# Optimization experiments

Measured on AMD Instinct MI355X. Metric: run time of the kernel, lower is better.

Reference implementation:

```python
import jax, jax.numpy as jnp
import numpy as np

B, C, H, S, E, NH, DD, DS = 16, 256, 1024, 1024, 512, 8, 512, 64
HD = E // NH               # head dim = 64
REL_MAX = 2048             # seq_len + prediction_length
S1 = S + 1                 # dyn tokens + 1 static token
NEG = jnp.float32(-1e9)


def setup_inputs() -> dict:
    key = jax.random.key(0)
    ks = jax.random.split(key, 24)
    rn = lambda k, shp, s=0.02: (jax.random.normal(k, shp, jnp.float32) * s)
    return {
        # forward tensor args
        "x":      jax.random.normal(ks[0], (B, C, H), jnp.float32),
        "dyn":    jax.random.normal(ks[1], (B, S, DD), jnp.float32),
        "static": jax.random.normal(ks[2], (B, DS), jnp.float32),
        # dynamic/static encoders (nn.Linear: y = x @ W.T + b)
        "dyn_W":  rn(ks[3], (E, DD)),  "dyn_b":  jnp.zeros((E,), jnp.float32),
        "stat_W": rn(ks[4], (E, DS)),  "stat_b": jnp.zeros((E,), jnp.float32),
        # static FiLM MLP: Linear(E,E) -> LeakyReLU(0.1) -> Linear(E,C) -> Tanh
        "film_W1": rn(ks[5], (E, E)), "film_b1": jnp.zeros((E,), jnp.float32),
        "film_W2": rn(ks[6], (C, E)), "film_b2": jnp.zeros((C,), jnp.float32),
        # query_proj: Conv1d(C->E, k=1)  (weight stored as [E, C])
        "q_W": rn(ks[7], (E, C)), "q_b": jnp.zeros((E,), jnp.float32),
        # MultiheadAttention packed in-proj [3E, E] and out-proj [E, E]
        "in_proj_W": rn(ks[8], (3 * E, E)), "in_proj_b": jnp.zeros((3 * E,), jnp.float32),
        "out_W": rn(ks[9], (E, E)), "out_b": jnp.zeros((E,), jnp.float32),
        # context_proj: Conv1d(E->C, k=1) (weight stored as [C, E])
        "ctx_W": rn(ks[10], (C, E)), "ctx_b": jnp.zeros((C,), jnp.float32),
        # learned relative-position bias table, size 2*REL_MAX-1
        "bias_table": rn(ks[11], (2 * REL_MAX - 1,)),
    }


def _leaky(v):
    return jnp.where(v >= 0, v, 0.1 * v)


def _attn_mask(bias_table):
    """Fused relative-position bias + causal mask, shape [H, S1]."""
    q_ids = jnp.arange(H)[:, None]           # [H,1]
    k_ids = jnp.arange(S1)[None, :]          # [1,S1]
    rel = jnp.clip(q_ids - k_ids, -REL_MAX + 1, REL_MAX - 1)
    bias = bias_table[rel + REL_MAX - 1]     # [H,S1]
    # dynamic tokens: query q may attend dyn token j only if j <= min(q, S-1);
    # last (static) token always visible
    allowed = jnp.minimum(q_ids, S - 1)
    blocked = (k_ids < S) & (k_ids > allowed)
    return bias + jnp.where(blocked, NEG, 0.0)


def reference(x, dyn, static, dyn_W, dyn_b, stat_W, stat_b,
              film_W1, film_b1, film_W2, film_b2, q_W, q_b,
              in_proj_W, in_proj_b, out_W, out_b, ctx_W, ctx_b, bias_table):
    # encoders
    dyn_tokens = dyn @ dyn_W.T + dyn_b                      # [B,S,E]
    static_token = static @ stat_W.T + stat_b               # [B,E]
    film = jnp.tanh(_leaky(static_token @ film_W1.T + film_b1) @ film_W2.T + film_b2)  # [B,C]
    cond_tokens = jnp.concatenate([dyn_tokens, static_token[:, None, :]], axis=1)      # [B,S1,E]

    # query_proj (1x1 conv) : [B,C,H] -> [B,H,E]
    query = jnp.einsum('bch,ec->bhe', x, q_W) + q_b

    # multi-head cross-attention with additive mask
    Wq, Wk, Wv = in_proj_W[:E], in_proj_W[E:2 * E], in_proj_W[2 * E:]
    bq, bk, bv = in_proj_b[:E], in_proj_b[E:2 * E], in_proj_b[2 * E:]
    q = (query @ Wq.T + bq).reshape(B, H, NH, HD).transpose(0, 2, 1, 3)        # [B,NH,H,HD]
    k = (cond_tokens @ Wk.T + bk).reshape(B, S1, NH, HD).transpose(0, 2, 1, 3)  # [B,NH,S1,HD]
    v = (cond_tokens @ Wv.T + bv).reshape(B, S1, NH, HD).transpose(0, 2, 1, 3)

    mask = _attn_mask(bias_table)                                               # [H,S1]
    scores = jnp.einsum('bnqd,bnkd->bnqk', q, k) / jnp.sqrt(jnp.float32(HD)) + mask
    attn = jax.nn.softmax(scores, axis=-1)
    ctx = jnp.einsum('bnqk,bnkd->bnqd', attn, v)                                # [B,NH,H,HD]
    ctx = ctx.transpose(0, 2, 1, 3).reshape(B, H, E) @ out_W.T + out_b          # [B,H,E]

    cond_context = jnp.swapaxes(ctx, 1, 2)                                      # [B,E,H]
    cond_residual = jnp.einsum('beh,ce->bch', cond_context, ctx_W) + ctx_b[None, :, None]
    scale = (1.0 + film)[:, :, None]                                            # FiLM [B,C,1]
    x_cond = (x + cond_residual) * scale                                        # == x*s + res*s
    return x_cond
```

## Files before the change

### kernel.cpp

```cpp
#include <hip/hip_runtime.h>
#include <cmath>

#define B_  16
#define C_  256
#define H_  1024
#define S_  1024
#define E_  512
#define NH_ 8
#define DD_ 512
#define DS_ 64
#define HD_ 64
#define S1_ 1025
#define RELM 2048
#define SV  1032

typedef __attribute__((ext_vector_type(8))) short bf16x8;
typedef __attribute__((ext_vector_type(4))) float f32x4;

__device__ __forceinline__ unsigned short f2bf(float f) {
    unsigned u = __float_as_uint(f);
    u += 0x7fffu + ((u >> 16) & 1u);
    return (unsigned short)(u >> 16);
}

#if __has_builtin(__builtin_amdgcn_exp2f)
#define EXP2F(x) __builtin_amdgcn_exp2f(x)
#else
#define EXP2F(x) exp2f(x)
#endif

__device__ __forceinline__ void gl2lds16(const unsigned short* g, unsigned short* l) {
#if __has_builtin(__builtin_amdgcn_global_load_lds)
    __builtin_amdgcn_global_load_lds(
        (const __attribute__((address_space(1))) void*)g,
        (__attribute__((address_space(3))) void*)l, 16, 0, 0);
#else
    const int ln = threadIdx.x & 63;
    *(bf16x8*)(l + ln * 8) = *(const bf16x8*)g;
#endif
}

__device__ __forceinline__ void conv8(const float* __restrict__ src,
                                      unsigned short* __restrict__ dst, int i) {
    float4 a = *(const float4*)(src + i);
    float4 b = *(const float4*)(src + i + 4);
    bf16x8 o;
    ((unsigned short*)&o)[0] = f2bf(a.x); ((unsigned short*)&o)[1] = f2bf(a.y);
    ((unsigned short*)&o)[2] = f2bf(a.z); ((unsigned short*)&o)[3] = f2bf(a.w);
    ((unsigned short*)&o)[4] = f2bf(b.x); ((unsigned short*)&o)[5] = f2bf(b.y);
    ((unsigned short*)&o)[6] = f2bf(b.z); ((unsigned short*)&o)[7] = f2bf(b.w);
    *(bf16x8*)(dst + i) = o;
}

__device__ __forceinline__ float wred(float p) {
#pragma unroll
    for (int off = 32; off; off >>= 1) p += __shfl_down(p, off, 64);
    return p;
}

#define U_DYN 1048576
#define U_KV  1114112
#define U_Q   1146880
#define U_TOT 1163264
__global__ __launch_bounds__(512)
void prep_conv(const float* __restrict__ dyn, unsigned short* __restrict__ dyn16,
               const float* __restrict__ ipW, unsigned short* __restrict__ ipWq16,
               unsigned short* __restrict__ ipWkv16,
               const float* __restrict__ ctxW, unsigned short* __restrict__ ctxW16,
               const float* __restrict__ statIn,
               const float* __restrict__ stat_W, const float* __restrict__ stat_b,
               float* __restrict__ st_g, unsigned short* __restrict__ st16)
{
    const int blk = blockIdx.x;
    const int t = threadIdx.x;
    if (blk < 512) {
        const float* ipWkv = ipW + (size_t)E_ * E_;
        const int stride = 512 * 512;
        for (int u = blk * 512 + t; u < U_TOT; u += stride) {
            if (u < U_DYN)      conv8(dyn,   dyn16,   u * 8);
            else if (u < U_KV)  conv8(ipWkv, ipWkv16, (u - U_DYN) * 8);
            else if (u < U_Q)   conv8(ipW,   ipWq16,  (u - U_KV) * 8);
            else                conv8(ctxW,  ctxW16,  (u - U_Q) * 8);
        }
    } else {
        const int sub = blk - 512;
        const int b = sub >> 2;
        const int q = sub & 3;
        const int wv = t >> 6;
        const int ln = t & 63;
        const float sv = statIn[b * DS_ + ln];
#pragma unroll 4
        for (int i = 0; i < 16; i++) {
            const int r = q * 128 + wv * 16 + i;
            const float p = wred(stat_W[(size_t)r * DS_ + ln] * sv);
            if (ln == 0) {
                const float v = p + stat_b[r];
                st_g[(size_t)b * E_ + r] = v;
                st16[(size_t)b * E_ + r] = f2bf(v);
            }
        }
    }
}

__global__ __launch_bounds__(512)
void prep_misc(const float* __restrict__ ipW, const float* __restrict__ ipb,
               const float* __restrict__ ctxW,
               const float* __restrict__ q_W, unsigned short* __restrict__ qWT16,
               const float* __restrict__ dynW, unsigned short* __restrict__ dynWT16,
               const float* __restrict__ outW, unsigned short* __restrict__ outWT16,
               const float* __restrict__ q_b, float* __restrict__ qb2,
               const float* __restrict__ dyn_b, float* __restrict__ bkv2,
               const float* __restrict__ out_b, const float* __restrict__ ctx_b,
               float* __restrict__ cb2,
               const float* __restrict__ st_g,
               const float* __restrict__ fW1, const float* __restrict__ fb1,
               float* __restrict__ h1_g)
{
    __shared__ float tle[64][65];
    const int blk = blockIdx.x;
    const int t = threadIdx.x;
    const float* ipWkv = ipW + (size_t)E_ * E_;
    const float* ipbkv = ipb + E_;

    if (blk < 128) {
        const int b   = blk >> 3;
        const int oct = blk & 7;
        const int wv  = t >> 6;
        const int ln  = t & 63;
        float str[8];
        *(float4*)&str[0] = *(const float4*)&st_g[(size_t)b * E_ + ln * 8];
        *(float4*)&str[4] = *(const float4*)&st_g[(size_t)b * E_ + ln * 8 + 4];
#pragma unroll 2
        for (int i = 0; i < 8; i++) {
            const int r = oct * 64 + wv * 8 + i;
            const float* wr = fW1 + (size_t)r * E_ + ln * 8;
            const float4 a = *(const float4*)wr;
            const float4 c = *(const float4*)(wr + 4);
            float p = a.x * str[0] + a.y * str[1] + a.z * str[2] + a.w * str[3]
                    + c.x * str[4] + c.y * str[5] + c.z * str[6] + c.w * str[7];
            p = wred(p);
            if (ln == 0) {
                const float v = p + fb1[r];
                h1_g[(size_t)b * E_ + r] = (v >= 0.f) ? v : 0.1f * v;
            }
        }
    } else if (blk < 352) {
        const int row = (blk - 128) * 8 + (t >> 6);
        const int ln  = t & 63;
        const float* src; const float* vec; float bias; float* dst;
        if (row < 512)       { src = ipW + (size_t)row * E_;            vec = q_b;   bias = ipb[row];        dst = qb2 + row; }
        else if (row < 1536) { const int n = row - 512;  src = ipWkv + (size_t)n * E_; vec = dyn_b; bias = ipbkv[n]; dst = bkv2 + n; }
        else                 { const int n = row - 1536; src = ctxW + (size_t)n * E_;  vec = out_b; bias = ctx_b[n]; dst = cb2 + n; }
        const float4 a  = *(const float4*)(src + ln * 8);
        const float4 c  = *(const float4*)(src + ln * 8 + 4);
        const float4 va = *(const float4*)(vec + ln * 8);
        const float4 vc = *(const float4*)(vec + ln * 8 + 4);
        float p = a.x * va.x + a.y * va.y + a.z * va.z + a.w * va.w
                + c.x * vc.x + c.y * vc.y + c.z * vc.z + c.w * vc.w;
        p = wred(p);
        if (ln == 0) *dst = p + bias;
    } else {
        const float* src; unsigned short* dst; int R, Cc, tile;
        const int tt = blk - 352;
        if (tt < 32)      { src = q_W;  dst = qWT16;   R = 512; Cc = 256; tile = tt; }
        else if (tt < 96) { src = dynW; dst = dynWT16; R = 512; Cc = 512; tile = tt - 32; }
        else              { src = outW; dst = outWT16; R = 512; Cc = 512; tile = tt - 96; }
        const int tpr = Cc / 64;
        const int r0 = (tile / tpr) * 64;
        const int c0 = (tile % tpr) * 64;
        const int tx = t & 15, ty = t >> 4;
#pragma unroll
        for (int i = 0; i < 2; i++) {
            const float4 v = *(const float4*)&src[(size_t)(r0 + ty + i * 32) * Cc + c0 + tx * 4];
            tle[ty + i * 32][tx * 4 + 0] = v.x;
            tle[ty + i * 32][tx * 4 + 1] = v.y;
            tle[ty + i * 32][tx * 4 + 2] = v.z;
            tle[ty + i * 32][tx * 4 + 3] = v.w;
        }
        __syncthreads();
#pragma unroll
        for (int i = 0; i < 2; i++) {
            const int cc = ty + i * 32;
            ushort4 o;
            o.x = f2bf(tle[tx * 4 + 0][cc]);
            o.y = f2bf(tle[tx * 4 + 1][cc]);
            o.z = f2bf(tle[tx * 4 + 2][cc]);
            o.w = f2bf(tle[tx * 4 + 3][cc]);
            *(ushort4*)&dst[(size_t)(c0 + cc) * R + r0 + tx * 4] = o;
        }
    }
}

__global__ __launch_bounds__(256)
void gemm_fold3(const unsigned short* __restrict__ ipWq16, const unsigned short* __restrict__ qWT16,
                unsigned short* __restrict__ WqW16,
                const unsigned short* __restrict__ ipWkv16, const unsigned short* __restrict__ dynWT16,
                unsigned short* __restrict__ Wkv216,
                const unsigned short* __restrict__ ctxW16, const unsigned short* __restrict__ outWT16,
                unsigned short* __restrict__ M216,
                const float* __restrict__ h1_g,
                const float* __restrict__ fW2, const float* __restrict__ fb2,
                float* __restrict__ scaleB)
{
    __shared__ unsigned short At[128 * 32];
    __shared__ unsigned short Wt[128 * 32];
    const int bid = blockIdx.x;
    const int tid  = threadIdx.x;
    if (bid >= 48) {
        const int sub = bid - 48;
        const int b = sub >> 2;
        const int q = sub & 3;
        const int wv = tid >> 6;
        const int ln = tid & 63;
        float h1r[8];
        *(float4*)&h1r[0] = *(const float4*)&h1_g[(size_t)b * E_ + ln * 8];
        *(float4*)&h1r[4] = *(const float4*)&h1_g[(size_t)b * E_ + ln * 8 + 4];
#pragma unroll 2
        for (int i = 0; i < 16; i++) {
            const int c = q * 64 + wv * 16 + i;
            const float* wr = fW2 + (size_t)c * E_ + ln * 8;
            const float4 a = *(const float4*)wr;
            const float4 cc = *(const float4*)(wr + 4);
            float p = a.x * h1r[0] + a.y * h1r[1] + a.z * h1r[2] + a.w * h1r[3]
                    + cc.x * h1r[4] + cc.y * h1r[5] + cc.z * h1r[6] + cc.w * h1r[7];
            p = wred(p);
            if (ln == 0) scaleB[b * C_ + c] = 1.f + tanhf(p + fb2[c]);
        }
        return;
    }
    const unsigned short *A, *W; unsigned short* O; int N, mb, nb;
    if (bid < 8)       { A = ipWq16;  W = qWT16;   O = WqW16;  N = 256; mb = bid >> 1;       nb = bid & 1; }
    else if (bid < 40) { A = ipWkv16; W = dynWT16; O = Wkv216; N = 512; mb = (bid - 8) >> 2; nb = (bid - 8) & 3; }
    else               { A = ctxW16;  W = outWT16; O = M216;   N = 512; mb = (bid - 40) >> 2; nb = (bid - 40) & 3; }
    const int m0 = mb * 128, n0 = nb * 128;

    const int wave = tid >> 6;
    const int lane = tid & 63;
    const int quad = lane >> 4;
    const int l15  = lane & 15;
    const int rw = (wave >> 1) * 64;
    const int cw = (wave & 1) * 64;
    const int srow = lane >> 2;
    const int scol = (lane & 3) * 8;

    f32x4 acc[4][4] = {};
    for (int k0 = 0; k0 < 512; k0 += 32) {
        __syncthreads();
#pragma unroll
        for (int c = 0; c < 2; c++) {
            const int chunk = wave + c * 4;
            gl2lds16(A + (size_t)(m0 + chunk * 16 + srow) * 512 + k0 + scol, &At[chunk * 512]);
            gl2lds16(W + (size_t)(n0 + chunk * 16 + srow) * 512 + k0 + scol, &Wt[chunk * 512]);
        }
        __syncthreads();
        bf16x8 af[4], wf[4];
#pragma unroll
        for (int i = 0; i < 4; i++)
            af[i] = *(const bf16x8*)&At[(rw + i * 16 + l15) * 32 + quad * 8];
#pragma unroll
        for (int j = 0; j < 4; j++)
            wf[j] = *(const bf16x8*)&Wt[(cw + j * 16 + l15) * 32 + quad * 8];
#pragma unroll
        for (int i = 0; i < 4; i++)
#pragma unroll
            for (int j = 0; j < 4; j++)
                acc[i][j] = __builtin_amdgcn_mfma_f32_16x16x32_bf16(af[i], wf[j], acc[i][j], 0, 0, 0);
    }
#pragma unroll
    for (int i = 0; i < 4; i++)
#pragma unroll
        for (int r = 0; r < 4; r++) {
            const int mm = m0 + rw + i * 16 + quad * 4 + r;
            unsigned short* cp = O + (size_t)mm * N + n0 + cw + l15;
#pragma unroll
            for (int j = 0; j < 4; j++)
                cp[j * 16] = f2bf(acc[i][j][r]);
        }
}

__global__ __launch_bounds__(256)
void xpose_kernel(const float* __restrict__ x, unsigned short* __restrict__ xT)
{
    __shared__ float t[64][65];
    const int b = blockIdx.z;
    const int h0 = blockIdx.x * 64;
    const int c0 = blockIdx.y * 64;
    const int tx = threadIdx.x & 15;
    const int ty = threadIdx.x >> 4;
#pragma unroll
    for (int i = 0; i < 4; i++) {
        const float4 v = *(const float4*)&x[((size_t)(b * C_ + c0 + ty + i * 16)) * H_ + h0 + tx * 4];
        t[ty + i * 16][tx * 4 + 0] = v.x;
        t[ty + i * 16][tx * 4 + 1] = v.y;
        t[ty + i * 16][tx * 4 + 2] = v.z;
        t[ty + i * 16][tx * 4 + 3] = v.w;
    }
    __syncthreads();
#pragma unroll
    for (int i = 0; i < 4; i++) {
        const int hh = ty + i * 16;
        ushort4 o;
        o.x = f2bf(t[tx * 4 + 0][hh]);
        o.y = f2bf(t[tx * 4 + 1][hh]);
        o.z = f2bf(t[tx * 4 + 2][hh]);
        o.w = f2bf(t[tx * 4 + 3][hh]);
        *(ushort4*)&xT[((size_t)(b * H_ + h0 + hh)) * C_ + c0 + tx * 4] = o;
    }
}

__global__ __launch_bounds__(256)
void gemm_qkv(const unsigned short* __restrict__ xT16, const unsigned short* __restrict__ WqW16,
              const float* __restrict__ qb2, unsigned short* __restrict__ q16,
              const unsigned short* __restrict__ dynA, const unsigned short* __restrict__ stA,
              const unsigned short* __restrict__ Wdyn, const unsigned short* __restrict__ Wst,
              const float* __restrict__ bdyn, const float* __restrict__ bst,
              unsigned short* __restrict__ k16, unsigned short* __restrict__ vtmp)
{
    __shared__ unsigned short At[2][128 * 32];
    __shared__ unsigned short Wt[2][128 * 32];
    const int bid0 = blockIdx.x;
    const int t = (bid0 & 7) * 193 + (bid0 >> 3);

    const int tid  = threadIdx.x;
    const int wave = tid >> 6;
    const int lane = tid & 63;
    const int quad = lane >> 4;
    const int l15  = lane & 15;
    const int rw = (wave >> 1) * 64;
    const int cw = (wave & 1) * 64;
    const int srow = lane >> 2;
    const int scol = (lane & 3) * 8;

    const unsigned short *A, *W;
    int m0, n0, K;
    bool isQ, stat = false;
    if (t < 1032) {
        const int y = t >> 3;
        stat = (y == 128);
        A = stat ? stA : dynA;
        W = stat ? Wst : Wdyn;
        m0 = stat ? 0 : y * 128;
        n0 = (t & 7) * 128;
        K = 512; isQ = false;
    } else {
        const int u = t - 1032;
        A = xT16; W = WqW16;
        m0 = (u >> 2) * 128;
        n0 = (u & 3) * 128;
        K = 256; isQ = true;
    }

    f32x4 acc[4][4] = {};
#pragma unroll
    for (int c = 0; c < 2; c++) {
        const int chunk = wave + c * 4;
        gl2lds16(A + (size_t)(m0 + chunk * 16 + srow) * K + scol, &At[0][chunk * 512]);
        gl2lds16(W + (size_t)(n0 + chunk * 16 + srow) * K + scol, &Wt[0][chunk * 512]);
    }
    int cur = 0;
    for (int k0 = 0; k0 < K; k0 += 32) {
        __syncthreads();
        if (k0 + 32 < K) {
            const int kn = k0 + 32;
#pragma unroll
            for (int c = 0; c < 2; c++) {
                const int chunk = wave + c * 4;
                gl2lds16(A + (size_t)(m0 + chunk * 16 + srow) * K + kn + scol, &At[cur ^ 1][chunk * 512]);
                gl2lds16(W + (size_t)(n0 + chunk * 16 + srow) * K + kn + scol, &Wt[cur ^ 1][chunk * 512]);
            }
        }
        bf16x8 af[4], wf[4];
#pragma unroll
        for (int i = 0; i < 4; i++)
            af[i] = *(const bf16x8*)&At[cur][(rw + i * 16 + l15) * 32 + quad * 8];
#pragma unroll
        for (int j = 0; j < 4; j++)
            wf[j] = *(const bf16x8*)&Wt[cur][(cw + j * 16 + l15) * 32 + quad * 8];
#pragma unroll
        for (int i = 0; i < 4; i++)
#pragma unroll
            for (int j = 0; j < 4; j++)
                acc[i][j] = __builtin_amdgcn_mfma_f32_16x16x32_bf16(af[i], wf[j], acc[i][j], 0, 0, 0);
        cur ^= 1;
    }

    if (isQ) {
        float bias4[4];
#pragma unroll
        for (int j = 0; j < 4; j++) bias4[j] = qb2[n0 + cw + j * 16 + l15];
#pragma unroll
        for (int i = 0; i < 4; i++) {
#pragma unroll
            for (int r = 0; r < 4; r++) {
                const int mm = m0 + rw + i * 16 + quad * 4 + r;
                unsigned short* cp = q16 + (size_t)mm * 512 + n0 + cw + l15;
#pragma unroll
                for (int j = 0; j < 4; j++)
                    cp[j * 16] = f2bf(acc[i][j][r] + bias4[j]);
            }
        }
    } else {
        const float* bias = stat ? bst : bdyn;
        const bool isV = (n0 >= 512);
        unsigned short* base = isV ? vtmp : k16;
        const int c0 = (isV ? n0 - 512 : n0) + cw + l15;
        float bias4[4];
#pragma unroll
        for (int j = 0; j < 4; j++) bias4[j] = bias[n0 + cw + j * 16 + l15];
#pragma unroll
        for (int i = 0; i < 4; i++) {
#pragma unroll
            for (int r = 0; r < 4; r++) {
                const int am = m0 + rw + i * 16 + quad * 4 + r;
                if (!stat || am < 16) {
                    const int orow = stat ? (am * S1_ + S_) : ((am >> 10) * S1_ + (am & 1023));
                    unsigned short* cp = base + (size_t)orow * 512 + c0;
#pragma unroll
                    for (int j = 0; j < 4; j++)
                        cp[j * 16] = f2bf(acc[i][j][r] + bias4[j]);
                }
            }
        }
    }
}

__global__ __launch_bounds__(256)
void gemm_final(const unsigned short* __restrict__ A, const unsigned short* __restrict__ W,
                const float* __restrict__ bias, float* __restrict__ Cout,
                const float* __restrict__ x, const float* __restrict__ scale)
{
    __shared__ unsigned short At[2][128 * 32];
    __shared__ unsigned short Wt[2][128 * 32];
    const int tid  = threadIdx.x;
    const int wave = tid >> 6;
    const int lane = tid & 63;
    const int quad = lane >> 4;
    const int l15  = lane & 15;
    const int m0 = blockIdx.y * 128;
    const int n0 = blockIdx.x * 128;
    const int rw = (wave >> 1) * 64;
    const int cw = (wave & 1) * 64;
    const int zb = blockIdx.z;
    const int K = E_;
    const unsigned short* Wb = W + (size_t)zb * H_ * E_;

    const int srow = lane >> 2;
    const int scol = (lane & 3) * 8;

    f32x4 acc[4][4] = {};
#pragma unroll
    for (int c = 0; c < 2; c++) {
        const int chunk = wave + c * 4;
        gl2lds16(A  + (size_t)(m0 + chunk * 16 + srow) * K + scol, &At[0][chunk * 512]);
        gl2lds16(Wb + (size_t)(n0 + chunk * 16 + srow) * K + scol, &Wt[0][chunk * 512]);
    }
    int cur = 0;
    for (int k0 = 0; k0 < K; k0 += 32) {
        __syncthreads();
        if (k0 + 32 < K) {
            const int kn = k0 + 32;
#pragma unroll
            for (int c = 0; c < 2; c++) {
                const int chunk = wave + c * 4;
                gl2lds16(A  + (size_t)(m0 + chunk * 16 + srow) * K + kn + scol, &At[cur ^ 1][chunk * 512]);
                gl2lds16(Wb + (size_t)(n0 + chunk * 16 + srow) * K + kn + scol, &Wt[cur ^ 1][chunk * 512]);
            }
        }
        bf16x8 af[4], wf[4];
#pragma unroll
        for (int i = 0; i < 4; i++)
            af[i] = *(const bf16x8*)&At[cur][(rw + i * 16 + l15) * 32 + quad * 8];
#pragma unroll
        for (int j = 0; j < 4; j++)
            wf[j] = *(const bf16x8*)&Wt[cur][(cw + j * 16 + l15) * 32 + quad * 8];
#pragma unroll
        for (int i = 0; i < 4; i++)
#pragma unroll
            for (int j = 0; j < 4; j++)
                acc[i][j] = __builtin_amdgcn_mfma_f32_16x16x32_bf16(af[i], wf[j], acc[i][j], 0, 0, 0);
        cur ^= 1;
    }

#pragma unroll
    for (int i = 0; i < 4; i++) {
#pragma unroll
        for (int r = 0; r < 4; r++) {
            const int mm = m0 + rw + i * 16 + quad * 4 + r;
            const float cb = bias[mm];
            const float sc = scale[zb * C_ + mm];
            const size_t base = ((size_t)(zb * C_ + mm)) * H_ + n0 + cw + l15;
#pragma unroll
            for (int j = 0; j < 4; j++)
                Cout[base + j * 16] = (x[base + j * 16] + acc[i][j][r] + cb) * sc;
        }
    }
}

__global__ __launch_bounds__(256)
void vtrans_kernel(const unsigned short* __restrict__ vtmp, unsigned short* __restrict__ vT)
{
    __shared__ unsigned short tle[64][72];
    const int b = blockIdx.z;
    const int s0 = blockIdx.x * 64;
    const int d0 = blockIdx.y * 64;
    const int tx = threadIdx.x & 15;
    const int ty = threadIdx.x >> 4;
#pragma unroll
    for (int i = 0; i < 4; i++) {
        const int s = s0 + ty + i * 16;
        ushort4 v = {0, 0, 0, 0};
        if (s < S1_)
            v = *(const ushort4*)&vtmp[((size_t)(b * S1_ + s)) * 512 + d0 + tx * 4];
        tle[ty + i * 16][tx * 4 + 0] = v.x;
        tle[ty + i * 16][tx * 4 + 1] = v.y;
        tle[ty + i * 16][tx * 4 + 2] = v.z;
        tle[ty + i * 16][tx * 4 + 3] = v.w;
    }
    __syncthreads();
    if (s0 + tx * 4 < SV) {
#pragma unroll
        for (int i = 0; i < 4; i++) {
            const int dd = ty + i * 16;
            ushort4 o;
            o.x = tle[tx * 4 + 0][dd];
            o.y = tle[tx * 4 + 1][dd];
            o.z = tle[tx * 4 + 2][dd];
            o.w = tle[tx * 4 + 3][dd];
            *(ushort4*)&vT[((size_t)(b * 512 + d0 + dd)) * SV + s0 + tx * 4] = o;
        }
    }
}

#define KS 72
#define VTS 40
#define PS 40

__global__ __launch_bounds__(256)
void attn_mfma_kernel(const unsigned short* __restrict__ q,
                      const unsigned short* __restrict__ k16,
                      const unsigned short* __restrict__ vT,
                      const float* __restrict__ bt,
                      unsigned short* __restrict__ ctx)
{
    const int blk  = blockIdx.x;
    const int qt   = 7 - (blk >> 7);
    const int pair = blk & 127;
    const int nh   = pair & 7;
    const int b    = pair >> 3;
    const int tid  = threadIdx.x;
    const int wave = tid >> 6;
    const int lane = tid & 63;
    const int quad = lane >> 4;
    const int l15  = lane & 15;
    const int q0w  = qt * 128 + wave * 32;

    __shared__ unsigned short Kt[32 * KS];
    __shared__ unsigned short VTl[64 * VTS];
    __shared__ unsigned short Pt[4][16 * PS];
    __shared__ float btl[2048];

    for (int i = tid; i < 2048; i += 256)
        btl[i] = (i < 1024) ? -1.0e9f : bt[1023 + i] * 1.442695041f;

    const float c2 = 0.125f * 1.442695041f;

    bf16x8 qa[2][2];
    const size_t qbase = ((size_t)(b * H_ + q0w)) * E_ + nh * HD_;
#pragma unroll
    for (int qf = 0; qf < 2; qf++)
#pragma unroll
        for (int ch = 0; ch < 2; ch++)
            qa[qf][ch] = *(const bf16x8*)(q + qbase + (size_t)(qf * 16 + l15) * E_ + ch * 32 + quad * 8);

    bf16x8 ones;
#pragma unroll
    for (int j = 0; j < 8; j++) ((short*)&ones)[j] = (short)0x3F80;

    f32x4 o[2][4] = {};
    f32x4 lf[2] = {};
    bf16x8 pa[2];

    const int srow = tid >> 3;
    const int scol = (tid & 7) * 8;
    const int frow = tid >> 2;
    const int fcol = (tid & 3) * 8;
    const unsigned short* kbase = k16 + (size_t)(b * S1_) * 512 + nh * HD_;
    const unsigned short* vrow = vT + ((size_t)(b * 512 + nh * HD_ + frow)) * SV;
    const int ntiles = 4 * qt + 5;
    const int wblk0 = (l15 >> 3);
    const int wsub  = (l15 & 7);
    const int rblk  = (quad ^ ((l15 >> 2) & 3)) << 3;

    bf16x8 kreg = *(const bf16x8*)(kbase + (size_t)srow * 512 + scol);
    bf16x8 vreg = *(const bf16x8*)(vrow + fcol);

    for (int t = 0; t < ntiles; t++) {
        const int k0 = (t == ntiles - 1) ? 1024 : t * 32;
        __syncthreads();
        {
            *(bf16x8*)&Kt[srow * KS + scol] = kreg;
            *(bf16x8*)&VTl[frow * VTS + fcol] = vreg;
        }
        __syncthreads();
        if (t + 1 < ntiles) {
            const int nk0 = (t + 1 == ntiles - 1) ? 1024 : (t + 1) * 32;
            kreg = *(const bf16x8*)(kbase + (size_t)(nk0 + srow) * 512 + scol);
            vreg = *(const bf16x8*)(vrow + nk0 + fcol);
        }

        f32x4 s[2][2] = {};
        __builtin_amdgcn_s_setprio(1);
#pragma unroll
        for (int ch = 0; ch < 2; ch++) {
            const bf16x8 kb0 = *(const bf16x8*)&Kt[l15 * KS + ch * 32 + quad * 8];
            const bf16x8 kb1 = *(const bf16x8*)&Kt[(16 + l15) * KS + ch * 32 + quad * 8];
            s[0][0] = __builtin_amdgcn_mfma_f32_16x16x32_bf16(qa[0][ch], kb0, s[0][0], 0, 0, 0);
            s[1][0] = __builtin_amdgcn_mfma_f32_16x16x32_bf16(qa[1][ch], kb0, s[1][0], 0, 0, 0);
            s[0][1] = __builtin_amdgcn_mfma_f32_16x16x32_bf16(qa[0][ch], kb1, s[0][1], 0, 0, 0);
            s[1][1] = __builtin_amdgcn_mfma_f32_16x16x32_bf16(qa[1][ch], kb1, s[1][1], 0, 0, 0);
        }
        __builtin_amdgcn_s_setprio(0);

        if (t != ntiles - 1) {
#pragma unroll
            for (int qf = 0; qf < 2; qf++) {
                unsigned short* pw = Pt[wave];
#pragma unroll
                for (int f = 0; f < 2; f++) {
                    const int base = q0w + qf * 16 + quad * 4 - (k0 + f * 16 + l15) + 1024;
                    const int cswz = ((f * 2 + wblk0) ^ quad) * 8 + wsub;
#pragma unroll
                    for (int r = 0; r < 4; r++) {
                        const float pp = EXP2F(s[qf][f][r] * c2 + btl[base + r]);
                        pw[(quad * 4 + r) * PS + cswz] = f2bf(pp);
                    }
                }
                pa[qf] = *(const bf16x8*)&pw[l15 * PS + rblk];
            }
        } else {
#pragma unroll
            for (int qf = 0; qf < 2; qf++) {
                unsigned short* pw = Pt[wave];
#pragma unroll
                for (int f = 0; f < 2; f++) {
                    const int kk = k0 + f * 16 + l15;
                    const int cswz = ((f * 2 + wblk0) ^ quad) * 8 + wsub;
#pragma unroll
                    for (int r = 0; r < 4; r++) {
                        const int qi = q0w + qf * 16 + quad * 4 + r;
                        const float pp = (kk == 1024)
                            ? __expf(s[qf][f][r] * 0.125f + bt[1023 + qi]) : 0.f;
                        pw[(quad * 4 + r) * PS + cswz] = f2bf(pp);
                    }
                }
                pa[qf] = *(const bf16x8*)&pw[l15 * PS + rblk];
            }
        }

        __builtin_amdgcn_s_setprio(1);
#pragma unroll
        for (int qf = 0; qf < 2; qf++)
            lf[qf] = __builtin_amdgcn_mfma_f32_16x16x32_bf16(pa[qf], ones, lf[qf], 0, 0, 0);
#pragma unroll
        for (int dt = 0; dt < 4; dt++) {
            const bf16x8 vb = *(const bf16x8*)&VTl[(dt * 16 + l15) * VTS + quad * 8];
#pragma unroll
            for (int qf = 0; qf < 2; qf++)
                o[qf][dt] = __builtin_amdgcn_mfma_f32_16x16x32_bf16(pa[qf], vb, o[qf][dt], 0, 0, 0);
        }
        __builtin_amdgcn_s_setprio(0);
    }

#pragma unroll
    for (int qf = 0; qf < 2; qf++) {
        unsigned short* crow = ctx + ((size_t)(b * H_ + q0w + qf * 16 + quad * 4)) * E_ + nh * HD_ + l15;
#pragma unroll
        for (int r = 0; r < 4; r++) {
            const float inv = 1.f / lf[qf][r];
#pragma unroll
            for (int dt = 0; dt < 4; dt++)
                crow[(size_t)r * E_ + dt * 16] = f2bf(o[qf][dt][r] * inv);
        }
    }
}

extern "C" void kernel_launch(void* const* d_in, const int* in_sizes, int n_in,
                              void* d_out, int out_size, void* d_ws, size_t ws_size,
                              hipStream_t stream)
{
    (void)in_sizes; (void)n_in; (void)out_size; (void)ws_size;
    const float* x      = (const float*)d_in[0];
    const float* dyn    = (const float*)d_in[1];
    const float* statIn = (const float*)d_in[2];
    const float* dyn_W  = (const float*)d_in[3];
    const float* dyn_b  = (const float*)d_in[4];
    const float* stat_W = (const float*)d_in[5];
    const float* stat_b = (const float*)d_in[6];
    const float* fW1    = (const float*)d_in[7];
    const float* fb1    = (const float*)d_in[8];
    const float* fW2    = (const float*)d_in[9];
    const float* fb2    = (const float*)d_in[10];
    const float* q_W    = (const float*)d_in[11];
    const float* q_b    = (const float*)d_in[12];
    const float* ipW    = (const float*)d_in[13];
    const float* ipb    = (const float*)d_in[14];
    const float* out_W  = (const float*)d_in[15];
    const float* out_b  = (const float*)d_in[16];
    const float* ctx_W  = (const float*)d_in[17];
    const float* ctx_b  = (const float*)d_in[18];
    const float* bt     = (const float*)d_in[19];
    float* out = (float*)d_out;
    const float* ipbkv = ipb + E_;

    const size_t KV_ROWS = 16512;
    char* w = (char*)d_ws; size_t off = 0;
    unsigned short* k16   = (unsigned short*)(w + off); off += KV_ROWS * 512 * 2;
    unsigned short* vtmp  = (unsigned short*)(w + off); off += KV_ROWS * 512 * 2;
    unsigned short* dyn16 = (unsigned short*)(w + off); off += (size_t)16 * 512 * SV * 2;
    unsigned short* q16   = (unsigned short*)(w + off); off += (size_t)B_ * H_ * E_ * 2;
    unsigned short* xT16  = (unsigned short*)(w + off); off += (size_t)B_ * H_ * C_ * 2;
    unsigned short* st16    = (unsigned short*)(w + off); off += (size_t)128 * E_ * 2;
    unsigned short* Wkv216  = (unsigned short*)(w + off); off += (size_t)1024 * 512 * 2;
    unsigned short* ipWkv16 = (unsigned short*)(w + off); off += (size_t)1024 * 512 * 2;
    unsigned short* ipWq16  = (unsigned short*)(w + off); off += (size_t)512 * 512 * 2;
    unsigned short* ctxW16  = (unsigned short*)(w + off); off += (size_t)256 * 512 * 2;
    unsigned short* qWT16   = (unsigned short*)(w + off); off += (size_t)256 * 512 * 2;
    unsigned short* dynWT16 = (unsigned short*)(w + off); off += (size_t)512 * 512 * 2;
    unsigned short* outWT16 = (unsigned short*)(w + off); off += (size_t)512 * 512 * 2;
    unsigned short* WqW16   = (unsigned short*)(w + off); off += (size_t)E_ * C_ * 2;
    unsigned short* M216    = (unsigned short*)(w + off); off += (size_t)C_ * E_ * 2;
    float* scaleB = (float*)(w + off); off += (size_t)B_ * C_ * 4;
    float* qb2    = (float*)(w + off); off += E_ * 4;
    float* bkv2   = (float*)(w + off); off += 1024 * 4;
    float* cb2    = (float*)(w + off); off += C_ * 4;
    float* st_g   = (float*)(w + off); off += (size_t)B_ * E_ * 4;
    float* h1_g   = (float*)(w + off); off += (size_t)B_ * E_ * 4;
    unsigned short* vT16  = dyn16;
    unsigned short* ctx16 = vtmp;

    prep_conv<<<576, 512, 0, stream>>>(dyn, dyn16, ipW, ipWq16, ipWkv16, ctx_W, ctxW16,
                                       statIn, stat_W, stat_b, st_g, st16);
    prep_misc<<<512, 512, 0, stream>>>(ipW, ipb, ctx_W, q_W, qWT16, dyn_W, dynWT16,
                                       out_W, outWT16, q_b, qb2, dyn_b, bkv2,
                                       out_b, ctx_b, cb2,
                                       st_g, fW1, fb1, h1_g);
    gemm_fold3<<<112, 256, 0, stream>>>(ipWq16, qWT16, WqW16,
                                        ipWkv16, dynWT16, Wkv216,
                                        ctxW16, outWT16, M216,
                                        h1_g, fW2, fb2, scaleB);
    xpose_kernel<<<dim3(H_ / 64, C_ / 64, B_), 256, 0, stream>>>(x, xT16);
    gemm_qkv<<<1544, 256, 0, stream>>>(xT16, WqW16, qb2, q16,
                                       dyn16, st16, Wkv216, ipWkv16, bkv2, ipbkv,
                                       k16, vtmp);
    vtrans_kernel<<<dim3(17, 8, B_), 256, 0, stream>>>(vtmp, vT16);
    attn_mfma_kernel<<<1024, 256, 0, stream>>>(q16, k16, vT16, bt, ctx16);
    gemm_final<<<dim3(H_ / 128, C_ / 128, B_), 256, 0, stream>>>(
        M216, ctx16, cb2, out, x, scaleB);
}
```

Measured before the change: 271.3 us.

## Fold x transpose into prep_conv and single-buffer gemm_final LDS tiles

The standalone x transpose/bf16 conversion kernel is merged into prep_conv as 1024 extra blocks of 512 threads, which removes one kernel launch and lets the transpose run alongside the weight conversion. Separately, gemm_final drops its double-buffered LDS prefetch and uses a single buffer with two barriers per k-step. That halves LDS use and may raise occupancy, but global loads no longer overlap with the MFMA work. The prep_conv blocks now all reserve the 64x65 float shared tile, including those that do not use it.

```diff
diff --git a/kernel.cpp b/kernel.cpp
--- a/kernel.cpp
+++ b/kernel.cpp
@@ -69,8 +69,10 @@
                const float* __restrict__ ctxW, unsigned short* __restrict__ ctxW16,
                const float* __restrict__ statIn,
                const float* __restrict__ stat_W, const float* __restrict__ stat_b,
-               float* __restrict__ st_g, unsigned short* __restrict__ st16)
+               float* __restrict__ st_g, unsigned short* __restrict__ st16,
+               const float* __restrict__ x, unsigned short* __restrict__ xT)
 {
+    __shared__ float tle[64][65];
     const int blk = blockIdx.x;
     const int t = threadIdx.x;
     if (blk < 512) {
@@ -82,7 +84,7 @@
             else if (u < U_Q)   conv8(ipW,   ipWq16,  (u - U_KV) * 8);
             else                conv8(ctxW,  ctxW16,  (u - U_Q) * 8);
         }
-    } else {
+    } else if (blk < 576) {
         const int sub = blk - 512;
         const int b = sub >> 2;
         const int q = sub & 3;
@@ -98,6 +100,31 @@
                 st_g[(size_t)b * E_ + r] = v;
                 st16[(size_t)b * E_ + r] = f2bf(v);
             }
+        }
+    } else {
+        const int sub = blk - 576;
+        const int b  = sub >> 6;
+        const int c0 = ((sub >> 4) & 3) * 64;
+        const int h0 = (sub & 15) * 64;
+        const int tx = t & 15, ty = t >> 4;
+#pragma unroll
+        for (int i = 0; i < 2; i++) {
+            const float4 v = *(const float4*)&x[((size_t)(b * C_ + c0 + ty + i * 32)) * H_ + h0 + tx * 4];
+            tle[ty + i * 32][tx * 4 + 0] = v.x;
+            tle[ty + i * 32][tx * 4 + 1] = v.y;
+            tle[ty + i * 32][tx * 4 + 2] = v.z;
+            tle[ty + i * 32][tx * 4 + 3] = v.w;
+        }
+        __syncthreads();
+#pragma unroll
+        for (int i = 0; i < 2; i++) {
+            const int hh = ty + i * 32;
+            ushort4 o;
+            o.x = f2bf(tle[tx * 4 + 0][hh]);
+            o.y = f2bf(tle[tx * 4 + 1][hh]);
+            o.z = f2bf(tle[tx * 4 + 2][hh]);
+            o.w = f2bf(tle[tx * 4 + 3][hh]);
+            *(ushort4*)&xT[((size_t)(b * H_ + h0 + hh)) * C_ + c0 + tx * 4] = o;
         }
     }
 }
@@ -279,36 +306,6 @@
 }
 
 __global__ __launch_bounds__(256)
-void xpose_kernel(const float* __restrict__ x, unsigned short* __restrict__ xT)
-{
-    __shared__ float t[64][65];
-    const int b = blockIdx.z;
-    const int h0 = blockIdx.x * 64;
-    const int c0 = blockIdx.y * 64;
-    const int tx = threadIdx.x & 15;
-    const int ty = threadIdx.x >> 4;
-#pragma unroll
-    for (int i = 0; i < 4; i++) {
-        const float4 v = *(const float4*)&x[((size_t)(b * C_ + c0 + ty + i * 16)) * H_ + h0 + tx * 4];
-        t[ty + i * 16][tx * 4 + 0] = v.x;
-        t[ty + i * 16][tx * 4 + 1] = v.y;
-        t[ty + i * 16][tx * 4 + 2] = v.z;
-        t[ty + i * 16][tx * 4 + 3] = v.w;
-    }
-    __syncthreads();
-#pragma unroll
-    for (int i = 0; i < 4; i++) {
-        const int hh = ty + i * 16;
-        ushort4 o;
-        o.x = f2bf(t[tx * 4 + 0][hh]);
-        o.y = f2bf(t[tx * 4 + 1][hh]);
-        o.z = f2bf(t[tx * 4 + 2][hh]);
-        o.w = f2bf(t[tx * 4 + 3][hh]);
-        *(ushort4*)&xT[((size_t)(b * H_ + h0 + hh)) * C_ + c0 + tx * 4] = o;
-    }
-}
-
-__global__ __launch_bounds__(256)
 void gemm_qkv(const unsigned short* __restrict__ xT16, const unsigned short* __restrict__ WqW16,
               const float* __restrict__ qb2, unsigned short* __restrict__ q16,
               const unsigned short* __restrict__ dynA, const unsigned short* __restrict__ stA,
@@ -429,8 +426,8 @@
                 const float* __restrict__ bias, float* __restrict__ Cout,
                 const float* __restrict__ x, const float* __restrict__ scale)
 {
-    __shared__ unsigned short At[2][128 * 32];
-    __shared__ unsigned short Wt[2][128 * 32];
+    __shared__ unsigned short At[128 * 32];
+    __shared__ unsigned short Wt[128 * 32];
     const int tid  = threadIdx.x;
     const int wave = tid >> 6;
     const int lane = tid & 63;
@@ -441,44 +438,34 @@
     const int rw = (wave >> 1) * 64;
     const int cw = (wave & 1) * 64;
     const int zb = blockIdx.z;
-    const int K = E_;
     const unsigned short* Wb = W + (size_t)zb * H_ * E_;
 
     const int srow = lane >> 2;
     const int scol = (lane & 3) * 8;
 
     f32x4 acc[4][4] = {};
-#pragma unroll
-    for (int c = 0; c < 2; c++) {
-        const int chunk = wave + c * 4;
-        gl2lds16(A  + (size_t)(m0 + chunk * 16 + srow) * K + scol, &At[0][chunk * 512]);
-        gl2lds16(Wb + (size_t)(n0 + chunk * 16 + srow) * K + scol, &Wt[0][chunk * 512]);
-    }
-    int cur = 0;
-    for (int k0 = 0; k0 < K; k0 += 32) {
-        __syncthreads();
-        if (k0 + 32 < K) {
-            const int kn = k0 + 32;
-#pragma unroll
-            for (int c = 0; c < 2; c++) {
-                const int chunk = wave + c * 4;
-                gl2lds16(A  + (size_t)(m0 + chunk * 16 + srow) * K + kn + scol, &At[cur ^ 1][chunk * 512]);
-                gl2lds16(Wb + (size_t)(n0 + chunk * 16 + srow) * K + kn + scol, &Wt[cur ^ 1][chunk * 512]);
-            }
-        }
+
+    for (int k0 = 0; k0 < E_; k0 += 32) {
+        __syncthreads();
+#pragma unroll
+        for (int c = 0; c < 2; c++) {
+            const int chunk = wave + c * 4;
+            gl2lds16(A  + (size_t)(m0 + chunk * 16 + srow) * E_ + k0 + scol, &At[chunk * 512]);
+            gl2lds16(Wb + (size_t)(n0 + chunk * 16 + srow) * E_ + k0 + scol, &Wt[chunk * 512]);
+        }
+        __syncthreads();
         bf16x8 af[4], wf[4];
 #pragma unroll
         for (int i = 0; i < 4; i++)
-            af[i] = *(const bf16x8*)&At[cur][(rw + i * 16 + l15) * 32 + quad * 8];
+            af[i] = *(const bf16x8*)&At[(rw + i * 16 + l15) * 32 + quad * 8];
 #pragma unroll
         for (int j = 0; j < 4; j++)
-            wf[j] = *(const bf16x8*)&Wt[cur][(cw + j * 16 + l15) * 32 + quad * 8];
+            wf[j] = *(const bf16x8*)&Wt[(cw + j * 16 + l15) * 32 + quad * 8];
 #pragma unroll
         for (int i = 0; i < 4; i++)
 #pragma unroll
             for (int j = 0; j < 4; j++)
                 acc[i][j] = __builtin_amdgcn_mfma_f32_16x16x32_bf16(af[i], wf[j], acc[i][j], 0, 0, 0);
-        cur ^= 1;
     }
 
 #pragma unroll
@@ -738,8 +725,8 @@
     unsigned short* vT16  = dyn16;
     unsigned short* ctx16 = vtmp;
 
-    prep_conv<<<576, 512, 0, stream>>>(dyn, dyn16, ipW, ipWq16, ipWkv16, ctx_W, ctxW16,
-                                       statIn, stat_W, stat_b, st_g, st16);
+    prep_conv<<<1600, 512, 0, stream>>>(dyn, dyn16, ipW, ipWq16, ipWkv16, ctx_W, ctxW16,
+                                        statIn, stat_W, stat_b, st_g, st16, x, xT16);
     prep_misc<<<512, 512, 0, stream>>>(ipW, ipb, ctx_W, q_W, qWT16, dyn_W, dynWT16,
                                        out_W, outWT16, q_b, qb2, dyn_b, bkv2,
                                        out_b, ctx_b, cb2,
@@ -748,7 +735,6 @@
                                         ipWkv16, dynWT16, Wkv216,
                                         ctxW16, outWT16, M216,
                                         h1_g, fW2, fb2, scaleB);
-    xpose_kernel<<<dim3(H_ / 64, C_ / 64, B_), 256, 0, stream>>>(x, xT16);
     gemm_qkv<<<1544, 256, 0, stream>>>(xT16, WqW16, qb2, q16,
                                        dyn16, st16, Wkv216, ipWkv16, bkv2, ipbkv,
                                        k16, vtmp);
```

New measurement: 265.0 us. 2.3% less time.
